# Kernel tuning notes

Hardware: AMD Instinct MI355X
Metric: run time of the kernel (lower is better)

Reference implementation:

```python
import jax, jax.numpy as jnp
import numpy as np

N = 50000      # nodes
E = 800000     # edges (avg degree 16)
F_IN = 128
H = 128
C = 2
EPS = 1e-5


def setup_inputs() -> dict:
    key = jax.random.key(0)
    ks = jax.random.split(key, 16)
    s_in = 1.0 / np.sqrt(F_IN)
    s_h = 1.0 / np.sqrt(H)
    return {
        "x": jax.random.normal(ks[0], (N, F_IN), jnp.float32),
        "edge_index": jax.random.randint(ks[1], (2, E), 0, N, jnp.int32),
        "W1": jax.random.normal(ks[2], (F_IN, H), jnp.float32) * s_in,
        "b1": jnp.zeros((H,), jnp.float32),
        "g1": jax.random.uniform(ks[3], (H,), jnp.float32, 0.5, 1.5),
        "be1": jnp.zeros((H,), jnp.float32),
        "m1": jax.random.normal(ks[4], (H,), jnp.float32) * 0.1,
        "v1": jax.random.uniform(ks[5], (H,), jnp.float32, 0.5, 1.5),
        "W2": jax.random.normal(ks[6], (H, H), jnp.float32) * s_h,
        "b2": jnp.zeros((H,), jnp.float32),
        "g2": jax.random.uniform(ks[7], (H,), jnp.float32, 0.5, 1.5),
        "be2": jnp.zeros((H,), jnp.float32),
        "m2": jax.random.normal(ks[8], (H,), jnp.float32) * 0.1,
        "v2": jax.random.uniform(ks[9], (H,), jnp.float32, 0.5, 1.5),
        "Wc": jax.random.normal(ks[10], (H, C), jnp.float32) * s_h,
        "bc": jnp.zeros((C,), jnp.float32),
    }


def _gcn_norm(edge_index):
    # Add self-loops: A_tilde = A + I, then symmetric normalization D^-1/2 A_tilde D^-1/2.
    loop = jnp.arange(N, dtype=edge_index.dtype)
    src = jnp.concatenate([edge_index[0], loop])
    dst = jnp.concatenate([edge_index[1], loop])
    deg = jax.ops.segment_sum(jnp.ones_like(src, jnp.float32), dst, num_segments=N)
    dinv = jnp.where(deg > 0, jax.lax.rsqrt(jnp.maximum(deg, 1.0)), 0.0)
    norm = dinv[src] * dinv[dst]  # per-edge coefficient
    return src, dst, norm


def _gcn_conv(h, src, dst, norm, W, b):
    h = h @ W                                  # [N, H]
    msg = h[src] * norm[:, None]               # gather + scale, [E+N, H]
    out = jax.ops.segment_sum(msg, dst, num_segments=N)
    return out + b


def _bn_eval(h, g, be, m, v):
    return (h - m) * (g * jax.lax.rsqrt(v + EPS)) + be


def reference(x, edge_index, W1, b1, g1, be1, m1, v1,
              W2, b2, g2, be2, m2, v2, Wc, bc):
    src, dst, norm = _gcn_norm(edge_index)
    h = _gcn_conv(x, src, dst, norm, W1, b1)
    h = jax.nn.relu(_bn_eval(h, g1, be1, m1, v1))  # dropout is identity in eval
    h = _gcn_conv(h, src, dst, norm, W2, b2)
    h = jax.nn.relu(_bn_eval(h, g2, be2, m2, v2))
    return h @ Wc + bc                            # logits [N, 2]
```

## Files before the change

kernel.cpp:

```cpp
#include <hip/hip_runtime.h>
#include <hip/hip_fp16.h>

#define EPSV 1e-5f
#define HSZ 6400
#define BPB 32

using half8 = __attribute__((ext_vector_type(8))) _Float16;
using f32x4 = __attribute__((ext_vector_type(4))) float;

__device__ __forceinline__ int bin_lo(int b, int mul) {
    return (int)((((long long)b << 25) + mul - 1) / mul);
}

__global__ __launch_bounds__(128) void k_setup(const float* __restrict__ W1, const float* __restrict__ W2,
                                               _Float16* __restrict__ whi1, _Float16* __restrict__ wlo1,
                                               _Float16* __restrict__ whi2, _Float16* __restrict__ wlo2,
                                               const float* __restrict__ g1, const float* __restrict__ v1,
                                               const float* __restrict__ b1, const float* __restrict__ m1,
                                               const float* __restrict__ be1,
                                               const float* __restrict__ g2, const float* __restrict__ v2,
                                               const float* __restrict__ b2, const float* __restrict__ m2,
                                               const float* __restrict__ be2,
                                               float* __restrict__ par, int* __restrict__ bcur) {
    int b = blockIdx.x;
    int t = threadIdx.x;
    if (b < 32) {
        const float* W = (b < 16) ? W1 : W2;
        _Float16* whi = (b < 16) ? whi1 : whi2;
        _Float16* wlo = (b < 16) ? wlo1 : wlo2;
        int tile = ((b & 15) << 1) | (t >> 6);
        int l = t & 63;
        int kt = tile >> 3, ct = tile & 7;
        int k0 = kt * 32 + (l >> 4) * 8;
        int c = ct * 16 + (l & 15);
        half8 hi, lo;
#pragma unroll
        for (int j = 0; j < 8; j++) {
            float w = W[(k0 + j) * 128 + c];
            _Float16 h = (_Float16)w;
            hi[j] = h;
            lo[j] = (_Float16)(w - (float)h);
        }
        size_t o = (size_t)tile * 64 + l;
        ((half8*)whi)[o] = hi;
        ((half8*)wlo)[o] = lo;
    } else {
        int c = t;
        float s1 = g1[c] * rsqrtf(v1[c] + EPSV);
        par[c] = s1;
        par[128 + c] = fmaf(b1[c] - m1[c], s1, be1[c]);
        float s2 = g2[c] * rsqrtf(v2[c] + EPSV);
        par[256 + c] = s2;
        par[384 + c] = fmaf(b2[c] - m2[c], s2, be2[c]);
        if (c < 8) bcur[c] = 0;
    }
}

__device__ __forceinline__ void bin_body(const int* __restrict__ src, const int* __restrict__ dst,
                                         int* __restrict__ bcur, unsigned int* __restrict__ binned,
                                         int E, int mul, int bin_cap, int bid, int nblocks, int tid) {
    int lane = tid & 63;
    int gw = (bid * 256 + tid) >> 6;
    int nw = (nblocks * 256) >> 6;
    bool v4 = ((E & 3) == 0);
    for (int base = gw * 1024; base < E; base += nw * 1024) {
        unsigned int vals[16];
        int bins[16];
        unsigned long long clo = 0, chi = 0;
#pragma unroll
        for (int g = 0; g < 4; g++) {
            int e0 = base + g * 256 + lane * 4;
            int4 s4, d4;
            if (v4 && e0 + 3 < E) {
                s4 = *(const int4*)(src + e0);
                d4 = *(const int4*)(dst + e0);
            } else {
                s4.x = (e0 < E) ? src[e0] : 0;         d4.x = (e0 < E) ? dst[e0] : -1;
                s4.y = (e0 + 1 < E) ? src[e0 + 1] : 0; d4.y = (e0 + 1 < E) ? dst[e0 + 1] : -1;
                s4.z = (e0 + 2 < E) ? src[e0 + 2] : 0; d4.z = (e0 + 2 < E) ? dst[e0 + 2] : -1;
                s4.w = (e0 + 3 < E) ? src[e0 + 3] : 0; d4.w = (e0 + 3 < E) ? dst[e0 + 3] : -1;
            }
            int ss[4] = {s4.x, s4.y, s4.z, s4.w};
            int dd[4] = {d4.x, d4.y, d4.z, d4.w};
#pragma unroll
            for (int k = 0; k < 4; k++) {
                int j = g * 4 + k;
                int d = dd[k];
                if (d >= 0) {
                    vals[j] = ((unsigned int)ss[k] << 16) | (unsigned int)d;
                    int b = (d * mul) >> 25;
                    bins[j] = b;
                    if (b < 4) clo += 1ull << (b * 16);
                    else       chi += 1ull << ((b - 4) * 16);
                } else bins[j] = -1;
            }
        }
        unsigned long long ilo = clo, ihi = chi;
#pragma unroll
        for (int d = 1; d < 64; d <<= 1) {
            unsigned long long ulo = __shfl_up(ilo, d, 64);
            unsigned long long uhi = __shfl_up(ihi, d, 64);
            if (lane >= d) { ilo += ulo; ihi += uhi; }
        }
        unsigned long long tlo = __shfl(ilo, 63, 64), thi = __shfl(ihi, 63, 64);
        unsigned long long plo = ilo - clo, phi = ihi - chi;
        int mytot = 0;
        if (lane < 4) mytot = (int)((tlo >> (lane * 16)) & 0xffff);
        else if (lane < 8) mytot = (int)((thi >> ((lane - 4) * 16)) & 0xffff);
        int alloc = 0;
        if (lane < 8) alloc = atomicAdd(&bcur[lane], mytot);
#pragma unroll
        for (int j = 0; j < 16; j++) {
            int b = bins[j];
            int bs = (b < 0) ? 0 : b;
            int bbase = __shfl(alloc, bs, 64);
            int sh = (bs & 3) * 16;
            unsigned long long sel = (bs < 4) ? plo : phi;
            int rel = (int)((sel >> sh) & 0xffffu);
            unsigned long long inc = 1ull << sh;
            if (bs < 4) plo += inc; else phi += inc;
            if (b >= 0) binned[(size_t)bs * bin_cap + bbase + rel] = vals[j];
        }
    }
}

__device__ __forceinline__ void gemm_body_f32(const float* __restrict__ A,
                                              const _Float16* __restrict__ whi,
                                              const _Float16* __restrict__ wlo,
                                              unsigned short* __restrict__ out, int M,
                                              int bid, int tid, uint4* __restrict__ sB) {
    int l = tid & 63;
    int w = tid >> 6;
    int r0 = bid * 64 + w * 16;
    int ra = r0 + (l & 15);
    if (ra >= M) ra = M - 1;
    int kl = (l >> 4) * 8;

    float4 af0[4], af1[4];
#pragma unroll
    for (int kt = 0; kt < 4; kt++) {
        const float* pa = A + (size_t)ra * 128 + kt * 32 + kl;
        af0[kt] = *(const float4*)pa;
        af1[kt] = *(const float4*)(pa + 4);
    }

    {
        const uint4* gh = (const uint4*)whi;
        const uint4* gl = (const uint4*)wlo;
#pragma unroll
        for (int i = 0; i < 8; i++) sB[tid + i * 256] = gh[tid + i * 256];
#pragma unroll
        for (int i = 0; i < 8; i++) sB[2048 + tid + i * 256] = gl[tid + i * 256];
    }
    __syncthreads();

    f32x4 acc[8];
#pragma unroll
    for (int i = 0; i < 8; i++) acc[i] = (f32x4)0.f;

    const half8* bh8 = (const half8*)sB;
    const half8* bl8 = (const half8*)(sB + 2048);

#pragma unroll
    for (int kt = 0; kt < 4; kt++) {
        half8 ah, al;
        float fa[8] = {af0[kt].x, af0[kt].y, af0[kt].z, af0[kt].w,
                       af1[kt].x, af1[kt].y, af1[kt].z, af1[kt].w};
#pragma unroll
        for (int j = 0; j < 8; j++) {
            _Float16 h = (_Float16)fa[j];
            ah[j] = h;
            al[j] = (_Float16)(fa[j] - (float)h);
        }
#pragma unroll
        for (int ct = 0; ct < 8; ct++) {
            half8 bh = bh8[(kt * 8 + ct) * 64 + l];
            half8 bl = bl8[(kt * 8 + ct) * 64 + l];
            acc[ct] = __builtin_amdgcn_mfma_f32_16x16x32_f16(ah, bh, acc[ct], 0, 0, 0);
            acc[ct] = __builtin_amdgcn_mfma_f32_16x16x32_f16(al, bh, acc[ct], 0, 0, 0);
            acc[ct] = __builtin_amdgcn_mfma_f32_16x16x32_f16(ah, bl, acc[ct], 0, 0, 0);
        }
    }

    __syncthreads();
    _Float16* stw = (_Float16*)sB + w * 2048;
#pragma unroll
    for (int r = 0; r < 4; r++) {
        int trow = (l >> 4) * 4 + r;
#pragma unroll
        for (int ct = 0; ct < 8; ct++)
            stw[trow * 128 + ct * 16 + (l & 15)] = (_Float16)(acc[ct][r]);
    }
#pragma unroll
    for (int p = 0; p < 4; p++) {
        int trow = p * 4 + (l >> 4);
        int grow = r0 + trow;
        if (grow < M) {
            uint4 v = *(const uint4*)&stw[trow * 128 + (l & 15) * 8];
            *(uint4*)&out[(size_t)grow * 128 + (l & 15) * 8] = v;
        }
    }
}

__global__ __launch_bounds__(256) void k_bingemm(const int* __restrict__ src, const int* __restrict__ dst,
                                                 int* __restrict__ bcur, unsigned int* __restrict__ binned,
                                                 int E, int mul, int bin_cap,
                                                 const float* __restrict__ x,
                                                 const _Float16* __restrict__ whi,
                                                 const _Float16* __restrict__ wlo,
                                                 unsigned short* __restrict__ outHs, int M, int bin_blocks) {
    __shared__ uint4 sB[4096];
    if ((int)blockIdx.x < bin_blocks) {
        bin_body(src, dst, bcur, binned, E, mul, bin_cap, blockIdx.x, bin_blocks, threadIdx.x);
        return;
    }
    gemm_body_f32(x, whi, wlo, outHs, M, blockIdx.x - bin_blocks, threadIdx.x, sB);
}

__global__ __launch_bounds__(256) void k_count(const unsigned int* __restrict__ binned,
                                               const int* __restrict__ bcnt, int* __restrict__ phist,
                                               int mul, int bin_cap) {
    __shared__ int hist[HSZ];
    int b = blockIdx.x & 7;
    int blk = blockIdx.x >> 3;
    int t = threadIdx.x;
    for (int i = t; i < HSZ; i += 256) hist[i] = 0;
    __syncthreads();
    int lo = bin_lo(b, mul);
    int cnt = bcnt[b];
    int e0 = (int)((long long)blk * cnt / BPB);
    int e1 = (int)((long long)(blk + 1) * cnt / BPB);
    const unsigned int* bp = binned + (size_t)b * bin_cap;
    for (int i = e0 + t; i < e1; i += 256) {
        int d = (int)(bp[i] & 0xffffu);
        atomicAdd(&hist[d - lo], 1);
    }
    __syncthreads();
    int* ph = phist + (size_t)blockIdx.x * HSZ;
    for (int i = t; i < HSZ; i += 256) ph[i] = hist[i];
}

__global__ __launch_bounds__(256) void k_bsum(int* __restrict__ phist, int* __restrict__ deg,
                                              int* __restrict__ bsum, int N, int mul) {
    int t = threadIdx.x;
    int base = blockIdx.x * 1024;
    int s = 0;
    for (int j = 0; j < 4; j++) {
        int i = base + j * 256 + t;
        if (i < N) {
            int b = (i * mul) >> 25;
            int lo = bin_lo(b, mul);
            int local = i - lo;
            int run = 0;
#pragma unroll
            for (int blk = 0; blk < BPB; blk++) {
                int* p = phist + (size_t)(blk * 8 + b) * HSZ + local;
                int c = *p;
                *p = run;
                run += c;
            }
            deg[i] = run;
            s += (run + 7) & ~7;
        }
    }
#pragma unroll
    for (int d = 1; d < 64; d <<= 1) s += __shfl_xor(s, d, 64);
    __shared__ int ws[4];
    if ((t & 63) == 0) ws[t >> 6] = s;
    __syncthreads();
    if (t == 0) bsum[blockIdx.x] = ws[0] + ws[1] + ws[2] + ws[3];
}

__global__ __launch_bounds__(256) void k_scanout(const int* __restrict__ deg, const int* __restrict__ bsum,
                                                 int* __restrict__ row_start, int* __restrict__ rend,
                                                 float* __restrict__ dinv, int n, int nb) {
    __shared__ int s_boff;
    __shared__ int ws[4];
    int t = threadIdx.x, lane = t & 63, wid = t >> 6;
    if (t < 64) {
        int v = (t < nb) ? bsum[t] : 0;
        int incl = v;
#pragma unroll
        for (int d = 1; d < 64; d <<= 1) {
            int u = __shfl_up(incl, d, 64);
            if (t >= d) incl += u;
        }
        if (t == (int)blockIdx.x) s_boff = incl - v;
    }
    __syncthreads();
    int base = blockIdx.x * 1024 + t * 4;
    int v[4], pv[4], ts = 0;
#pragma unroll
    for (int j = 0; j < 4; j++) {
        v[j] = (base + j < n) ? deg[base + j] : 0;
        pv[j] = (v[j] + 7) & ~7;
        ts += pv[j];
    }
    int incl = ts;
#pragma unroll
    for (int d = 1; d < 64; d <<= 1) {
        int u = __shfl_up(incl, d, 64);
        if (lane >= d) incl += u;
    }
    if (lane == 63) ws[wid] = incl;
    __syncthreads();
    int wo = 0;
    for (int i = 0; i < wid; i++) wo += ws[i];
    int run = s_boff + wo + (incl - ts);
#pragma unroll
    for (int j = 0; j < 4; j++) {
        if (base + j < n) {
            row_start[base + j] = run;
            rend[base + j] = run + v[j];
            dinv[base + j] = rsqrtf((float)v[j] + 1.0f);
            run += pv[j];
        }
    }
}

__global__ __launch_bounds__(256) void k_fill(const unsigned int* __restrict__ binned,
                                              const int* __restrict__ bcnt, const int* __restrict__ row_start,
                                              const int* __restrict__ phist, const float* __restrict__ dinv,
                                              unsigned int* __restrict__ csr,
                                              int N, int mul, int bin_cap) {
    __shared__ int cur[HSZ];
    int b = blockIdx.x & 7;
    int blk = blockIdx.x >> 3;
    int t = threadIdx.x;
    int lo = bin_lo(b, mul);
    int hi = (b == 7) ? N : bin_lo(b + 1, mul);
    if (hi > N) hi = N;
    const int* ph = phist + (size_t)blockIdx.x * HSZ;
    for (int i = t; i < HSZ; i += 256) {
        int d = lo + i;
        cur[i] = (d < hi) ? (row_start[d] + ph[i]) : 0;
    }
    __syncthreads();
    int cnt = bcnt[b];
    int e0 = (int)((long long)blk * cnt / BPB);
    int e1 = (int)((long long)(blk + 1) * cnt / BPB);
    const unsigned int* bp = binned + (size_t)b * bin_cap;
    for (int i = e0 + t; i < e1; i += 256) {
        unsigned int v = bp[i];
        int d = (int)(v & 0xffffu);
        int s = (int)(v >> 16);
        __half h = __float2half_rn(dinv[s]);
        unsigned short hb = *(unsigned short*)&h;
        int q = atomicAdd(&cur[d - lo], 1);
        csr[q] = ((unsigned int)hb << 16) | (unsigned int)s;
    }
}

__device__ __forceinline__ void f2fma(float2& a, const __half2 h, float w) {
    float2 f = __half22float2(h);
    a.x = fmaf(f.x, w, a.x);
    a.y = fmaf(f.y, w, a.y);
}

__device__ __forceinline__ float pk_w(unsigned int pk) {
    __half h;
    *(unsigned short*)&h = (unsigned short)(pk >> 16);
    return __half2float(h);
}

__device__ __forceinline__ void aggr_gather1(const float4* __restrict__ Hs4, const unsigned int* __restrict__ csr,
                                             int rs, int re, int node, float dn, int lc, float2 acc[4]) {
    {
        float4 sv = Hs4[(size_t)node * 16 + lc];
        const __half2* h = (const __half2*)&sv;
        float2 f0 = __half22float2(h[0]), f1 = __half22float2(h[1]);
        float2 f2 = __half22float2(h[2]), f3 = __half22float2(h[3]);
        acc[0] = make_float2(f0.x * dn, f0.y * dn);
        acc[1] = make_float2(f1.x * dn, f1.y * dn);
        acc[2] = make_float2(f2.x * dn, f2.y * dn);
        acc[3] = make_float2(f3.x * dn, f3.y * dn);
    }
    int nch = (re - rs + 7) >> 3;
    if (nch <= 0) return;
    float2 accB[4] = {{0.f, 0.f}, {0.f, 0.f}, {0.f, 0.f}, {0.f, 0.f}};
    const uint4* cp = (const uint4*)(csr + rs);
    uint4 q0 = cp[0], q1 = cp[1];
    for (int c = 0; c < nch; c++) {
        uint4 n0 = q0, n1 = q1;
        if (c + 1 < nch) { n0 = cp[2 * c + 2]; n1 = cp[2 * c + 3]; }
        unsigned int pks[8] = {q0.x, q0.y, q0.z, q0.w, q1.x, q1.y, q1.z, q1.w};
        int base = rs + c * 8;
        float4 v[8];
        float w[8];
#pragma unroll
        for (int j = 0; j < 8; j++) {
            unsigned int pk = (base + j < re) ? pks[j] : 0u;
            w[j] = pk_w(pk);
            v[j] = Hs4[(size_t)(pk & 0xffffu) * 16 + lc];
        }
#pragma unroll
        for (int j = 0; j < 8; j++) {
            const __half2* h = (const __half2*)&v[j];
            float2* acp = (j & 1) ? accB : acc;
            f2fma(acp[0], h[0], w[j]);
            f2fma(acp[1], h[1], w[j]);
            f2fma(acp[2], h[2], w[j]);
            f2fma(acp[3], h[3], w[j]);
        }
        q0 = n0; q1 = n1;
    }
#pragma unroll
    for (int k = 0; k < 4; k++) {
        acc[k].x += accB[k].x;
        acc[k].y += accB[k].y;
    }
}

__device__ __forceinline__ void bn_relu(const float2 acc[4], float dn, const float* __restrict__ par,
                                        int lc, float4& y0, float4& y1) {
    float4 s0 = ((const float4*)par)[lc * 2];
    float4 s1 = ((const float4*)par)[lc * 2 + 1];
    float4 t0 = ((const float4*)par)[32 + lc * 2];
    float4 t1 = ((const float4*)par)[32 + lc * 2 + 1];
    y0.x = fmaxf(fmaf(acc[0].x * dn, s0.x, t0.x), 0.f);
    y0.y = fmaxf(fmaf(acc[0].y * dn, s0.y, t0.y), 0.f);
    y0.z = fmaxf(fmaf(acc[1].x * dn, s0.z, t0.z), 0.f);
    y0.w = fmaxf(fmaf(acc[1].y * dn, s0.w, t0.w), 0.f);
    y1.x = fmaxf(fmaf(acc[2].x * dn, s1.x, t1.x), 0.f);
    y1.y = fmaxf(fmaf(acc[2].y * dn, s1.y, t1.y), 0.f);
    y1.z = fmaxf(fmaf(acc[3].x * dn, s1.z, t1.z), 0.f);
    y1.w = fmaxf(fmaf(acc[3].y * dn, s1.w, t1.w), 0.f);
}

__global__ __launch_bounds__(512, 4) void k_aggr_gemm(const float4* __restrict__ Hs4,
                                                      const int* __restrict__ row_start,
                                                      const int* __restrict__ rend,
                                                      const unsigned int* __restrict__ csr,
                                                      const float* __restrict__ dinv,
                                                      const float* __restrict__ par,
                                                      const _Float16* __restrict__ whi,
                                                      const _Float16* __restrict__ wlo,
                                                      unsigned short* __restrict__ outHs2, int n) {
    __shared__ uint4 sB[2048];
    __shared__ _Float16 sA[32 * 128];
    int t = threadIdx.x;

    {
        const uint4* gh = (const uint4*)whi;
        sB[t] = gh[t];
        sB[t + 512] = gh[t + 512];
        sB[t + 1024] = gh[t + 1024];
        sB[t + 1536] = gh[t + 1536];
    }

    int lc = t & 15;
    int nl = t >> 4;
    int node = blockIdx.x * 32 + nl;
    float4 y0 = make_float4(0.f, 0.f, 0.f, 0.f);
    float4 y1 = make_float4(0.f, 0.f, 0.f, 0.f);
    if (node < n) {
        float dn = dinv[node];
        float2 acc[4];
        aggr_gather1(Hs4, csr, row_start[node], rend[node], node, dn, lc, acc);
        bn_relu(acc, dn, par, lc, y0, y1);
    }
    {
        half8 av;
        av[0] = (_Float16)y0.x; av[1] = (_Float16)y0.y; av[2] = (_Float16)y0.z; av[3] = (_Float16)y0.w;
        av[4] = (_Float16)y1.x; av[5] = (_Float16)y1.y; av[6] = (_Float16)y1.z; av[7] = (_Float16)y1.w;
        int tile = ((nl >> 4) << 2) | (lc >> 2);
        int fl = ((lc & 3) << 4) | (nl & 15);
        ((half8*)sA)[tile * 64 + fl] = av;
    }
    __syncthreads();

    int w = t >> 6, l = t & 63;
    const half8* bh8 = (const half8*)sB;
    const half8* gl8 = (const half8*)wlo;
    const half8* aF = (const half8*)sA;
    f32x4 accT[2];
#pragma unroll
    for (int tt = 0; tt < 2; tt++) {
        int tile = w * 2 + tt;
        int rt = tile >> 3, ct = tile & 7;
        half8 bl[4];
#pragma unroll
        for (int kt = 0; kt < 4; kt++) bl[kt] = gl8[(kt * 8 + ct) * 64 + l];
        f32x4 acc = (f32x4)0.f;
#pragma unroll
        for (int kt = 0; kt < 4; kt++) {
            half8 a = aF[(rt * 4 + kt) * 64 + l];
            half8 bh = bh8[(kt * 8 + ct) * 64 + l];
            acc = __builtin_amdgcn_mfma_f32_16x16x32_f16(a, bh, acc, 0, 0, 0);
            acc = __builtin_amdgcn_mfma_f32_16x16x32_f16(a, bl[kt], acc, 0, 0, 0);
        }
        accT[tt] = acc;
    }
    __syncthreads();

#pragma unroll
    for (int tt = 0; tt < 2; tt++) {
        int tile = w * 2 + tt;
        int rt = tile >> 3, ct = tile & 7;
#pragma unroll
        for (int r = 0; r < 4; r++) {
            int row = rt * 16 + (l >> 4) * 4 + r;
            sA[row * 128 + ct * 16 + (l & 15)] = (_Float16)(accT[tt][r]);
        }
    }
    __syncthreads();

    {
        int row = t >> 4;
        int grow = blockIdx.x * 32 + row;
        if (grow < n) {
            uint4 v = *(const uint4*)&sA[row * 128 + (t & 15) * 8];
            *(uint4*)&outHs2[(size_t)grow * 128 + (t & 15) * 8] = v;
        }
    }
}

__device__ __forceinline__ void aggr_gather2(const float4* __restrict__ Hs4, const unsigned int* __restrict__ csr,
                                             int rs, int re, int node, float dn, int lc, float2 acc[4]) {
    {
        float4 sv = Hs4[(size_t)node * 16 + lc];
        const __half2* h = (const __half2*)&sv;
        float2 f0 = __half22float2(h[0]), f1 = __half22float2(h[1]);
        float2 f2 = __half22float2(h[2]), f3 = __half22float2(h[3]);
        acc[0] = make_float2(f0.x * dn, f0.y * dn);
        acc[1] = make_float2(f1.x * dn, f1.y * dn);
        acc[2] = make_float2(f2.x * dn, f2.y * dn);
        acc[3] = make_float2(f3.x * dn, f3.y * dn);
    }
    int nch = (re - rs + 7) >> 3;
    if (nch <= 0) return;
    float2 accB[4] = {{0.f, 0.f}, {0.f, 0.f}, {0.f, 0.f}, {0.f, 0.f}};
    const uint4* cp = (const uint4*)(csr + rs);
    uint4 qa0 = cp[0], qa1 = cp[1];
    uint4 qb0 = cp[2], qb1 = cp[3];
    for (int c = 0; c < nch; c += 2) {
        uint4 na0 = qa0, na1 = qa1, nb0 = qb0, nb1 = qb1;
        if (c + 2 < nch) { na0 = cp[2 * c + 4]; na1 = cp[2 * c + 5]; nb0 = cp[2 * c + 6]; nb1 = cp[2 * c + 7]; }
        unsigned int pA[8] = {qa0.x, qa0.y, qa0.z, qa0.w, qa1.x, qa1.y, qa1.z, qa1.w};
        unsigned int pB[8] = {qb0.x, qb0.y, qb0.z, qb0.w, qb1.x, qb1.y, qb1.z, qb1.w};
        int baseA = rs + c * 8;
        int baseB = baseA + 8;
        float4 vA[8], vB[8];
        float wA[8], wB[8];
#pragma unroll
        for (int j = 0; j < 8; j++) {
            unsigned int pk = (baseA + j < re) ? pA[j] : 0u;
            wA[j] = pk_w(pk);
            vA[j] = Hs4[(size_t)(pk & 0xffffu) * 16 + lc];
        }
#pragma unroll
        for (int j = 0; j < 8; j++) {
            unsigned int pk = (baseB + j < re) ? pB[j] : 0u;
            wB[j] = pk_w(pk);
            vB[j] = Hs4[(size_t)(pk & 0xffffu) * 16 + lc];
        }
#pragma unroll
        for (int j = 0; j < 8; j++) {
            const __half2* h = (const __half2*)&vA[j];
            float2* acp = (j & 1) ? accB : acc;
            f2fma(acp[0], h[0], wA[j]);
            f2fma(acp[1], h[1], wA[j]);
            f2fma(acp[2], h[2], wA[j]);
            f2fma(acp[3], h[3], wA[j]);
        }
#pragma unroll
        for (int j = 0; j < 8; j++) {
            const __half2* h = (const __half2*)&vB[j];
            float2* acp = (j & 1) ? accB : acc;
            f2fma(acp[0], h[0], wB[j]);
            f2fma(acp[1], h[1], wB[j]);
            f2fma(acp[2], h[2], wB[j]);
            f2fma(acp[3], h[3], wB[j]);
        }
        qa0 = na0; qa1 = na1; qb0 = nb0; qb1 = nb1;
    }
#pragma unroll
    for (int k = 0; k < 4; k++) {
        acc[k].x += accB[k].x;
        acc[k].y += accB[k].y;
    }
}

__global__ __launch_bounds__(256) void k_aggr_cls(const float4* __restrict__ Hs4, const int* __restrict__ row_start,
                                                  const int* __restrict__ rend,
                                                  const unsigned int* __restrict__ csr, const float* __restrict__ dinv,
                                                  const float* __restrict__ par, const float4* __restrict__ Wc4,
                                                  const float* __restrict__ bc, float2* __restrict__ out, int n) {
    int lc = threadIdx.x & 15;
    int node = blockIdx.x * 16 + (threadIdx.x >> 4);
    if (node >= n) return;
    float dn = dinv[node];
    float2 acc[4];
    aggr_gather2(Hs4, csr, row_start[node], rend[node], node, dn, lc, acc);
    float4 y0, y1;
    bn_relu(acc, dn, par, lc, y0, y1);
    float4 w0 = Wc4[lc * 4], w1 = Wc4[lc * 4 + 1], w2 = Wc4[lc * 4 + 2], w3 = Wc4[lc * 4 + 3];
    float p0 = y0.x * w0.x + y0.y * w0.z + y0.z * w1.x + y0.w * w1.z
             + y1.x * w2.x + y1.y * w2.z + y1.z * w3.x + y1.w * w3.z;
    float p1 = y0.x * w0.y + y0.y * w0.w + y0.z * w1.y + y0.w * w1.w
             + y1.x * w2.y + y1.y * w2.w + y1.z * w3.y + y1.w * w3.w;
#pragma unroll
    for (int d = 1; d < 16; d <<= 1) {
        p0 += __shfl_xor(p0, d, 16);
        p1 += __shfl_xor(p1, d, 16);
    }
    if (lc == 0) out[node] = make_float2(p0 + bc[0], p1 + bc[1]);
}

extern "C" void kernel_launch(void* const* d_in, const int* in_sizes, int n_in,
                              void* d_out, int out_size, void* d_ws, size_t ws_size,
                              hipStream_t stream) {
    const float* x = (const float*)d_in[0];
    const int* ei = (const int*)d_in[1];
    const float* W1 = (const float*)d_in[2];
    const float* b1 = (const float*)d_in[3];
    const float* g1 = (const float*)d_in[4];
    const float* be1 = (const float*)d_in[5];
    const float* m1 = (const float*)d_in[6];
    const float* v1 = (const float*)d_in[7];
    const float* W2 = (const float*)d_in[8];
    const float* b2 = (const float*)d_in[9];
    const float* g2 = (const float*)d_in[10];
    const float* be2 = (const float*)d_in[11];
    const float* m2 = (const float*)d_in[12];
    const float* v2 = (const float*)d_in[13];
    const float* Wc = (const float*)d_in[14];
    const float* bc = (const float*)d_in[15];
    float* out = (float*)d_out;

    const int N = in_sizes[0] / 128;
    const int E = in_sizes[1] / 2;
    const int* src = ei;
    const int* dst = ei + E;

    const int mul = (int)((8LL << 25) / N);
    const int bin_cap = ((E / 8 + 8192 + 63) / 64) * 64;

    int* W = (int*)d_ws;
    size_t off = 0;
    int* deg = W + off; off += N;
    int* bcur = W + off; off += 8;
    int* row_start = W + off; off += (size_t)N + 1;
    int* rend = W + off; off += N;
    float* dinv = (float*)(W + off); off += N;
    int* bsum = W + off; off += 64;
    float* par = (float*)(W + off); off += 512;
    _Float16* whi1 = (_Float16*)(W + off); off += 8192;
    _Float16* wlo1 = (_Float16*)(W + off); off += 8192;
    _Float16* whi2 = (_Float16*)(W + off); off += 8192;
    _Float16* wlo2 = (_Float16*)(W + off); off += 8192;
    int* phist = W + off; off += (size_t)8 * BPB * HSZ;
    unsigned int* csr = (unsigned int*)(W + off); off += (size_t)E + 8 * N + 64;
    unsigned int* binned = (unsigned int*)(W + off); off += (size_t)8 * bin_cap;
    off = (off + 3) & ~(size_t)3;
    __half* Hs = (__half*)(W + off); off += (size_t)N * 64;
    __half* Hs2 = (__half*)(W + off);

    k_setup<<<33, 128, 0, stream>>>(W1, W2, whi1, wlo1, whi2, wlo2,
                                    g1, v1, b1, m1, be1, g2, v2, b2, m2, be2,
                                    par, bcur);

    int nb = (N + 1023) / 1024;
    int gbm = (N + 63) / 64;
    int bin_blocks = 512;
    k_bingemm<<<bin_blocks + gbm, 256, 0, stream>>>(src, dst, bcur, binned, E, mul, bin_cap,
                                                    x, whi1, wlo1, (unsigned short*)Hs, N, bin_blocks);
    k_count<<<8 * BPB, 256, 0, stream>>>(binned, bcur, phist, mul, bin_cap);
    k_bsum<<<nb, 256, 0, stream>>>(phist, deg, bsum, N, mul);
    k_scanout<<<nb, 256, 0, stream>>>(deg, bsum, row_start, rend, dinv, N, nb);
    k_fill<<<8 * BPB, 256, 0, stream>>>(binned, bcur, row_start, phist, dinv, csr, N, mul, bin_cap);

    int gba = (N + 31) / 32;
    k_aggr_gemm<<<gba, 512, 0, stream>>>((const float4*)Hs, row_start, rend, csr, dinv, par,
                                         whi2, wlo2, (unsigned short*)Hs2, N);
    int ab = (N + 15) / 16;
    k_aggr_cls<<<ab, 256, 0, stream>>>((const float4*)Hs2, row_start, rend, csr, dinv, par + 256,
                                       (const float4*)Wc, bc, (float2*)out, N);
}
```

Measured before the change: 145.0 us.

## Group nodes by in-degree via counting-sort permutation to balance aggregation work

```diff
diff --git a/kernel.cpp b/kernel.cpp
--- a/kernel.cpp
+++ b/kernel.cpp
@@ -21,7 +21,8 @@
                                                const float* __restrict__ g2, const float* __restrict__ v2,
                                                const float* __restrict__ b2, const float* __restrict__ m2,
                                                const float* __restrict__ be2,
-                                               float* __restrict__ par, int* __restrict__ bcur) {
+                                               float* __restrict__ par, int* __restrict__ bcur,
+                                               int* __restrict__ dh, int* __restrict__ dcur) {
     int b = blockIdx.x;
     int t = threadIdx.x;
     if (b < 32) {
@@ -53,6 +54,7 @@
         par[256 + c] = s2;
         par[384 + c] = fmaf(b2[c] - m2[c], s2, be2[c]);
         if (c < 8) bcur[c] = 0;
+        if (c < 64) { dh[c] = 0; dcur[c] = 0; }
     }
 }
 
@@ -241,8 +243,12 @@
 }
 
 __global__ __launch_bounds__(256) void k_bsum(int* __restrict__ phist, int* __restrict__ deg,
-                                              int* __restrict__ bsum, int N, int mul) {
+                                              int* __restrict__ bsum, int* __restrict__ dh,
+                                              int N, int mul) {
+    __shared__ int dhist[64];
     int t = threadIdx.x;
+    if (t < 64) dhist[t] = 0;
+    __syncthreads();
     int base = blockIdx.x * 1024;
     int s = 0;
     for (int j = 0; j < 4; j++) {
@@ -260,6 +266,7 @@
                 run += c;
             }
             deg[i] = run;
+            atomicAdd(&dhist[run < 63 ? run : 63], 1);
             s += (run + 7) & ~7;
         }
     }
@@ -269,11 +276,13 @@
     if ((t & 63) == 0) ws[t >> 6] = s;
     __syncthreads();
     if (t == 0) bsum[blockIdx.x] = ws[0] + ws[1] + ws[2] + ws[3];
+    if (t < 64 && dhist[t]) atomicAdd(&dh[t], dhist[t]);
 }
 
 __global__ __launch_bounds__(256) void k_scanout(const int* __restrict__ deg, const int* __restrict__ bsum,
                                                  int* __restrict__ row_start, int* __restrict__ rend,
-                                                 float* __restrict__ dinv, int n, int nb) {
+                                                 float* __restrict__ dinv, const int* __restrict__ dh,
+                                                 int* __restrict__ dstart, int n, int nb) {
     __shared__ int s_boff;
     __shared__ int ws[4];
     int t = threadIdx.x, lane = t & 63, wid = t >> 6;
@@ -286,6 +295,16 @@
             if (t >= d) incl += u;
         }
         if (t == (int)blockIdx.x) s_boff = incl - v;
+        if (blockIdx.x == 0) {
+            int dv = dh[t];
+            int di = dv;
+#pragma unroll
+            for (int d = 1; d < 64; d <<= 1) {
+                int u = __shfl_up(di, d, 64);
+                if (t >= d) di += u;
+            }
+            dstart[t] = di - dv;
+        }
     }
     __syncthreads();
     int base = blockIdx.x * 1024 + t * 4;
@@ -315,6 +334,17 @@
             dinv[base + j] = rsqrtf((float)v[j] + 1.0f);
             run += pv[j];
         }
+    }
+}
+
+__global__ __launch_bounds__(256) void k_dscatter(const int* __restrict__ deg, const int* __restrict__ dstart,
+                                                  int* __restrict__ dcur, int* __restrict__ perm, int N) {
+    int i = blockIdx.x * 256 + threadIdx.x;
+    if (i < N) {
+        int b = deg[i];
+        if (b > 63) b = 63;
+        int p = atomicAdd(&dcur[b], 1);
+        perm[dstart[b] + p] = i;
     }
 }
 
@@ -435,6 +465,7 @@
                                                       const float* __restrict__ par,
                                                       const _Float16* __restrict__ whi,
                                                       const _Float16* __restrict__ wlo,
+                                                      const int* __restrict__ perm,
                                                       unsigned short* __restrict__ outHs2, int n) {
     __shared__ uint4 sB[2048];
     __shared__ _Float16 sA[32 * 128];
@@ -450,10 +481,11 @@
 
     int lc = t & 15;
     int nl = t >> 4;
-    int node = blockIdx.x * 32 + nl;
+    int idx = blockIdx.x * 32 + nl;
+    int node = (idx < n) ? perm[idx] : -1;
     float4 y0 = make_float4(0.f, 0.f, 0.f, 0.f);
     float4 y1 = make_float4(0.f, 0.f, 0.f, 0.f);
-    if (node < n) {
+    if (node >= 0) {
         float dn = dinv[node];
         float2 acc[4];
         aggr_gather1(Hs4, csr, row_start[node], rend[node], node, dn, lc, acc);
@@ -507,8 +539,9 @@
 
     {
         int row = t >> 4;
-        int grow = blockIdx.x * 32 + row;
-        if (grow < n) {
+        int oidx = blockIdx.x * 32 + row;
+        if (oidx < n) {
+            int grow = perm[oidx];
             uint4 v = *(const uint4*)&sA[row * 128 + (t & 15) * 8];
             *(uint4*)&outHs2[(size_t)grow * 128 + (t & 15) * 8] = v;
         }
@@ -585,10 +618,12 @@
                                                   const int* __restrict__ rend,
                                                   const unsigned int* __restrict__ csr, const float* __restrict__ dinv,
                                                   const float* __restrict__ par, const float4* __restrict__ Wc4,
-                                                  const float* __restrict__ bc, float2* __restrict__ out, int n) {
+                                                  const float* __restrict__ bc, const int* __restrict__ perm,
+                                                  float2* __restrict__ out, int n) {
     int lc = threadIdx.x & 15;
-    int node = blockIdx.x * 16 + (threadIdx.x >> 4);
-    if (node >= n) return;
+    int idx = blockIdx.x * 16 + (threadIdx.x >> 4);
+    if (idx >= n) return;
+    int node = perm[idx];
     float dn = dinv[node];
     float2 acc[4];
     aggr_gather2(Hs4, csr, row_start[node], rend[node], node, dn, lc, acc);
@@ -640,6 +675,10 @@
     size_t off = 0;
     int* deg = W + off; off += N;
     int* bcur = W + off; off += 8;
+    int* dh = W + off; off += 64;
+    int* dcur = W + off; off += 64;
+    int* dstart = W + off; off += 64;
+    int* perm = W + off; off += N;
     int* row_start = W + off; off += (size_t)N + 1;
     int* rend = W + off; off += N;
     float* dinv = (float*)(W + off); off += N;
@@ -658,7 +697,7 @@
 
     k_setup<<<33, 128, 0, stream>>>(W1, W2, whi1, wlo1, whi2, wlo2,
                                     g1, v1, b1, m1, be1, g2, v2, b2, m2, be2,
-                                    par, bcur);
+                                    par, bcur, dh, dcur);
 
     int nb = (N + 1023) / 1024;
     int gbm = (N + 63) / 64;
@@ -666,14 +705,15 @@
     k_bingemm<<<bin_blocks + gbm, 256, 0, stream>>>(src, dst, bcur, binned, E, mul, bin_cap,
                                                     x, whi1, wlo1, (unsigned short*)Hs, N, bin_blocks);
     k_count<<<8 * BPB, 256, 0, stream>>>(binned, bcur, phist, mul, bin_cap);
-    k_bsum<<<nb, 256, 0, stream>>>(phist, deg, bsum, N, mul);
-    k_scanout<<<nb, 256, 0, stream>>>(deg, bsum, row_start, rend, dinv, N, nb);
+    k_bsum<<<nb, 256, 0, stream>>>(phist, deg, bsum, dh, N, mul);
+    k_scanout<<<nb, 256, 0, stream>>>(deg, bsum, row_start, rend, dinv, dh, dstart, N, nb);
+    k_dscatter<<<(N + 255) / 256, 256, 0, stream>>>(deg, dstart, dcur, perm, N);
     k_fill<<<8 * BPB, 256, 0, stream>>>(binned, bcur, row_start, phist, dinv, csr, N, mul, bin_cap);
 
     int gba = (N + 31) / 32;
     k_aggr_gemm<<<gba, 512, 0, stream>>>((const float4*)Hs, row_start, rend, csr, dinv, par,
-                                         whi2, wlo2, (unsigned short*)Hs2, N);
+                                         whi2, wlo2, perm, (unsigned short*)Hs2, N);
     int ab = (N + 15) / 16;
     k_aggr_cls<<<ab, 256, 0, stream>>>((const float4*)Hs2, row_start, rend, csr, dinv, par + 256,
-                                       (const float4*)Wc, bc, (float2*)out, N);
-}
+                                       (const float4*)Wc, bc, perm, (float2*)out, N);
+}
```

New measurement: 299.1 us. +106.3%, slower.
